# Performance work log

Hardware: AMD Instinct MI355X
Metric: run time of the kernel (lower is better)

Reference implementation:

```python
import jax, jax.numpy as jnp
import numpy as np

N_DRUG = 20000; N_DIS = 20000; E_G = 320000
B = 4096; N_MOL = 65536; E_MOL = 262144
IN = 128; H = 256; OUT = 128; NF = 9; V = 128
EPS = 1e-5


def _bn(x, g, b):
    # BatchNorm1d in training mode: batch statistics (biased var), eps=1e-5
    m = jnp.mean(x, 0); v = jnp.var(x, 0)
    return g * (x - m) * jax.lax.rsqrt(v + EPS) + b


def _gcn_conv(x, W, b, src, dst, n):
    # PyG GCNConv: add self-loops, sym-normalized aggregation of x@W, + bias
    h = x @ W  # [n, out]
    deg = jnp.ones((n,), x.dtype).at[dst].add(jnp.ones(src.shape, x.dtype))  # deg incl. self-loop
    dinv = jax.lax.rsqrt(deg)
    msg = (dinv[src] * dinv[dst])[:, None] * h[src]  # [E, out]
    out = (h / deg[:, None]).at[dst].add(msg)  # self-loop norm = 1/deg
    return out + b


def _gcn(x, Ws, bs, gs, betas, edge_index, n):
    src, dst = edge_index[0], edge_index[1]
    for i in range(len(Ws) - 1):
        x = jax.nn.relu(_bn(_gcn_conv(x, Ws[i], bs[i], src, dst, n), gs[i], betas[i]))
    return _gcn_conv(x, Ws[-1], bs[-1], src, dst, n)


def _conv_block(x, W, b, g, beta):
    # Conv1d(k=3,s=1,p=1) -> MaxPool1d(2,2) -> BatchNorm1d -> ReLU
    y = jax.lax.conv_general_dilated(x, W, (1,), ((1, 1),), dimension_numbers=('NCH', 'OIH', 'NCH')) + b[None, :, None]
    y = jax.lax.reduce_window(y, -jnp.inf, jax.lax.max, (1, 1, 2), (1, 1, 2), 'VALID')
    m = jnp.mean(y, (0, 2)); v = jnp.var(y, (0, 2))
    y = g[None, :, None] * (y - m[None, :, None]) * jax.lax.rsqrt(v + EPS)[None, :, None] + beta[None, :, None]
    return jax.nn.relu(y)


def setup_inputs() -> dict:
    key = jax.random.key(0)
    ks = iter(jax.random.split(key, 64))
    def nrm(shape, s=0.05):
        return jax.random.normal(next(ks), shape, jnp.float32) * s
    inp = {}
    inp['drug_x'] = nrm((N_DRUG, IN), 1.0)
    inp['drug_edge_index'] = jax.random.randint(next(ks), (2, E_G), 0, N_DRUG)
    inp['drug_idx'] = jax.random.randint(next(ks), (B,), 0, N_DRUG)
    inp['dis_x'] = nrm((N_DIS, IN), 1.0)
    inp['dis_edge_index'] = jax.random.randint(next(ks), (2, E_G), 0, N_DIS)
    inp['dis_idx'] = jax.random.randint(next(ks), (B,), 0, N_DIS)
    inp['mol_x'] = jax.random.randint(next(ks), (N_MOL, NF), 0, V)
    inp['mol_edge_index'] = jax.random.randint(next(ks), (2, E_MOL), 0, N_MOL)
    inp['mol_batch'] = jnp.sort(jax.random.randint(next(ks), (N_MOL,), 0, B))
    for p in ['dr', 'di']:
        inp[p + '_W0'] = nrm((IN, H)); inp[p + '_W1'] = nrm((H, H)); inp[p + '_W2'] = nrm((H, OUT))
        inp[p + '_b0'] = jnp.zeros((H,)); inp[p + '_b1'] = jnp.zeros((H,)); inp[p + '_b2'] = jnp.zeros((OUT,))
        inp[p + '_g0'] = jnp.ones((H,)); inp[p + '_g1'] = jnp.ones((H,))
        inp[p + '_be0'] = jnp.zeros((H,)); inp[p + '_be1'] = jnp.zeros((H,))
    inp['mol_emb'] = nrm((NF, V, H))
    inp['mo_W0'] = nrm((H, H)); inp['mo_W1'] = nrm((H, H)); inp['mo_W2'] = nrm((H, OUT))
    inp['mo_b0'] = jnp.zeros((H,)); inp['mo_b1'] = jnp.zeros((H,)); inp['mo_b2'] = jnp.zeros((OUT,))
    inp['mo_g0'] = jnp.ones((H,)); inp['mo_g1'] = jnp.ones((H,))
    inp['mo_be0'] = jnp.zeros((H,)); inp['mo_be1'] = jnp.zeros((H,))
    inp['c1_W'] = nrm((6, 3, 3), 0.2); inp['c1_b'] = jnp.zeros((6,)); inp['c1_g'] = jnp.ones((6,)); inp['c1_be'] = jnp.zeros((6,))
    inp['c2_W'] = nrm((6, 6, 3), 0.2); inp['c2_b'] = jnp.zeros((6,)); inp['c2_g'] = jnp.ones((6,)); inp['c2_be'] = jnp.zeros((6,))
    inp['l1_W'] = nrm((192, 128)); inp['l1_b'] = jnp.zeros((128,))
    inp['l2_W'] = nrm((128, 1)); inp['l2_b'] = jnp.zeros((1,))
    return inp


def reference(drug_x, drug_edge_index, drug_idx, dis_x, dis_edge_index, dis_idx, mol_x, mol_edge_index, mol_batch,
              dr_W0, dr_W1, dr_W2, dr_b0, dr_b1, dr_b2, dr_g0, dr_g1, dr_be0, dr_be1,
              di_W0, di_W1, di_W2, di_b0, di_b1, di_b2, di_g0, di_g1, di_be0, di_be1,
              mol_emb, mo_W0, mo_W1, mo_W2, mo_b0, mo_b1, mo_b2, mo_g0, mo_g1, mo_be0, mo_be1,
              c1_W, c1_b, c1_g, c1_be, c2_W, c2_b, c2_g, c2_be, l1_W, l1_b, l2_W, l2_b):
    dfeat = _gcn(drug_x, [dr_W0, dr_W1, dr_W2], [dr_b0, dr_b1, dr_b2], [dr_g0, dr_g1], [dr_be0, dr_be1], drug_edge_index, N_DRUG)
    sfeat = _gcn(dis_x, [di_W0, di_W1, di_W2], [di_b0, di_b1, di_b2], [di_g0, di_g1], [di_be0, di_be1], dis_edge_index, N_DIS)
    # AtomEncoder: sum of per-feature categorical embeddings -> [N_MOL, H]
    h = jnp.sum(mol_emb[jnp.arange(NF)[None, :], mol_x], axis=1)
    mfeat = _gcn(h, [mo_W0, mo_W1, mo_W2], [mo_b0, mo_b1, mo_b2], [mo_g0, mo_g1], [mo_be0, mo_be1], mol_edge_index, N_MOL)
    mpool = jax.ops.segment_sum(mfeat, mol_batch, num_segments=B)  # global_add_pool
    fea = jnp.concatenate([dfeat[drug_idx], mpool, sfeat[dis_idx]], axis=1).reshape(B, 3, OUT)
    fea = _conv_block(fea, c1_W, c1_b, c1_g, c1_be)
    fea = _conv_block(fea, c2_W, c2_b, c2_g, c2_be)
    fea = fea.reshape(B, -1)  # [B, 192]
    fea = jax.nn.relu(fea @ l1_W + l1_b)
    return fea @ l2_W + l2_b
```

## Files before the change

kernel.cpp:

```cpp
#include <hip/hip_runtime.h>
#include <hip/hip_bf16.h>

#define N_DRUG 20000
#define N_DIS  20000
#define E_G    320000
#define BATCH  4096
#define N_MOL  65536
#define E_MOL  262144
#define NF     9
#define NV     128
#define DH     256
#define SPAN_P 20096
#define NP     40192
#define NTOT   105728
#define ETOT   902144

typedef short s16x8 __attribute__((ext_vector_type(8)));
typedef unsigned short u16x8 __attribute__((ext_vector_type(8)));
typedef float f32x4 __attribute__((ext_vector_type(4)));

typedef __attribute__((address_space(1))) const void gvoid_t;
typedef __attribute__((address_space(3))) void lvoid_t;

__device__ __forceinline__ float bfu2f(unsigned short u) {
    return __uint_as_float(((unsigned int)u) << 16);
}
__device__ __forceinline__ unsigned short f2bfu(float f) {
    __hip_bfloat16 b = __float2bfloat16(f);
    return *reinterpret_cast<unsigned short*>(&b);
}
__device__ __forceinline__ void atomAddF(float* p, float v) { unsafeAtomicAdd(p, v); }

__global__ void k_sentinel(float* out, int n, float v) {
    int i = blockIdx.x * 256 + threadIdx.x;
    if (i < n) out[i] = v;
}

__global__ void k_cast_pair(const float* __restrict__ a, const float* __restrict__ b,
                            unsigned short* __restrict__ out) {
    int i4 = blockIdx.x * 256 + threadIdx.x;
    if (i4 >= NP * 32) return;
    int row = i4 >> 5, c4 = (i4 & 31) * 4;
    float4 v = {0.f, 0.f, 0.f, 0.f};
    if (row < N_DRUG) v = *reinterpret_cast<const float4*>(a + (size_t)row * 128 + c4);
    else if (row >= SPAN_P && row < SPAN_P + N_DIS)
        v = *reinterpret_cast<const float4*>(b + (size_t)(row - SPAN_P) * 128 + c4);
    ushort4 o = {f2bfu(v.x), f2bfu(v.y), f2bfu(v.z), f2bfu(v.w)};
    *reinterpret_cast<ushort4*>(out + (size_t)row * 128 + c4) = o;
}

__global__ void k_wcast3(const float* __restrict__ W0, const float* __restrict__ W1,
                         const float* __restrict__ W2,
                         unsigned short* __restrict__ T0, unsigned short* __restrict__ T1,
                         unsigned short* __restrict__ T2, int Cin) {
    int i = blockIdx.x * 256 + threadIdx.x;
    int t0 = Cin * 256, t1 = 256 * 256, t2 = 256 * 128;
    if (i < t0) {
        int k = i / 256, c = i - k * 256;
        T0[(size_t)c * Cin + k] = f2bfu(W0[i]);
    } else if (i < t0 + t1) {
        int e = i - t0;
        int k = e / 256, c = e - k * 256;
        T1[(size_t)c * 256 + k] = f2bfu(W1[e]);
    } else if (i < t0 + t1 + t2) {
        int e = i - t0 - t1;
        int k = e / 128, c = e - k * 128;
        T2[(size_t)c * 256 + k] = f2bfu(W2[e]);
    }
}

__global__ void k_count3(const int* __restrict__ eA, const int* __restrict__ eB,
                         const int* __restrict__ eC, int* __restrict__ cnt) {
    int e = blockIdx.x * 256 + threadIdx.x;
    if (e >= ETOT) return;
    int d;
    if (e < E_G) d = eA[E_G + e];
    else if (e < 2 * E_G) d = eB[E_G + (e - E_G)] + SPAN_P;
    else d = eC[E_MOL + (e - 2 * E_G)] + NP;
    atomicAdd(&cnt[d], 1);
}

__global__ void k_scan1(const int* __restrict__ cnt, int* __restrict__ rowStart,
                        int* __restrict__ bsum, float* __restrict__ dinv, int n) {
    __shared__ int sh[256];
    int i = blockIdx.x * 256 + threadIdx.x;
    int v = (i < n) ? cnt[i] : 0;
    if (i < n) dinv[i] = rsqrtf(1.0f + (float)v);
    sh[threadIdx.x] = v;
    __syncthreads();
    for (int off = 1; off < 256; off <<= 1) {
        int t = (threadIdx.x >= off) ? sh[threadIdx.x - off] : 0;
        __syncthreads();
        sh[threadIdx.x] += t;
        __syncthreads();
    }
    if (i < n) rowStart[i] = sh[threadIdx.x] - v;
    if (threadIdx.x == 255) bsum[blockIdx.x] = sh[255];
}
__global__ void k_scan2b(int* __restrict__ bsum, int nb) {
    __shared__ int sh[256];
    __shared__ int carry;
    int t = threadIdx.x;
    if (t == 0) carry = 0;
    __syncthreads();
    for (int c0 = 0; c0 < nb; c0 += 256) {
        int v = (c0 + t < nb) ? bsum[c0 + t] : 0;
        sh[t] = v;
        __syncthreads();
        for (int off = 1; off < 256; off <<= 1) {
            int u = (t >= off) ? sh[t - off] : 0;
            __syncthreads();
            sh[t] += u;
            __syncthreads();
        }
        if (c0 + t < nb) bsum[c0 + t] = carry + sh[t] - v;
        __syncthreads();
        if (t == 0) carry += sh[255];
        __syncthreads();
    }
}
__global__ void k_scan3(int* __restrict__ rowStart, int* __restrict__ cursor,
                        const int* __restrict__ bsum, int n, int E) {
    int i = blockIdx.x * 256 + threadIdx.x;
    if (i < n) {
        int r = rowStart[i] + bsum[blockIdx.x];
        rowStart[i] = r;
        cursor[i] = r;
    }
    if (i == 0) rowStart[n] = E;
}
__global__ void k_fill3(const int* __restrict__ eA, const int* __restrict__ eB,
                        const int* __restrict__ eC, const float* __restrict__ dinv,
                        int* __restrict__ cursor, int2* __restrict__ csr2) {
    int e = blockIdx.x * 256 + threadIdx.x;
    if (e >= ETOT) return;
    int s, d;
    if (e < E_G) { s = eA[e]; d = eA[E_G + e]; }
    else if (e < 2 * E_G) { int i = e - E_G; s = eB[i] + SPAN_P; d = eB[E_G + i] + SPAN_P; }
    else { int i = e - 2 * E_G; s = eC[i] + NP; d = eC[E_MOL + i] + NP; }
    int p = atomicAdd(&cursor[d], 1);
    csr2[p] = make_int2(s, __float_as_int(dinv[s] * dinv[d]));
}

template<int AFFINE, int STATS>
__global__ __launch_bounds__(256) void k_gemm_mfma(const unsigned short* __restrict__ A,
                                                   const unsigned short* __restrict__ Bt0,
                                                   const unsigned short* __restrict__ Bt1,
                                                   const unsigned short* __restrict__ Bt2,
                                                   const float* __restrict__ coef,
                                                   unsigned short* __restrict__ Cout,
                                                   float* __restrict__ bnbuf,
// ... 55 lines not shown
            }
        }
    };

    f32x4 acc[4][4];
#pragma unroll
    for (int fm = 0; fm < 4; ++fm)
#pragma unroll
        for (int fn = 0; fn < 4; ++fn) acc[fm][fn] = f32x4{0.f, 0.f, 0.f, 0.f};

    stage(0, 0);
    __syncthreads();
    int nk = Kg >> 5;
    for (int t = 0; t < nk; ++t) {
        int cur = t & 1;
        if (t + 1 < nk) stage(cur ^ 1, (t + 1) * 32);
        s16x8 a[4], b[4];
#pragma unroll
        for (int fm = 0; fm < 4; ++fm)
            a[fm] = *reinterpret_cast<const s16x8*>(&Al[cur][kg][wrow + fm * 16 + lr][0]);
        if (AFFINE) {
            int k0 = t * 32;
            float sc[8], sh[8];
#pragma unroll
            for (int e = 0; e < 8; ++e) {
                sc[e] = csc[k0 + kg * 8 + e];
                sh[e] = csh[k0 + kg * 8 + e];
            }
#pragma unroll
            for (int fm = 0; fm < 4; ++fm)
#pragma unroll
                for (int e = 0; e < 8; ++e) {
                    float f = bfu2f((unsigned short)a[fm][e]);
                    a[fm][e] = (short)f2bfu(fmaxf(fmaf(sc[e], f, sh[e]), 0.f));
                }
        }
#pragma unroll
        for (int fn = 0; fn < 4; ++fn)
            b[fn] = *reinterpret_cast<const s16x8*>(&Bl[cur][kg][wcol + fn * 16 + lr][0]);
#pragma unroll
        for (int fm = 0; fm < 4; ++fm)
#pragma unroll
            for (int fn = 0; fn < 4; ++fn)
                acc[fm][fn] = __builtin_amdgcn_mfma_f32_16x16x32_bf16(a[fm], b[fn], acc[fm][fn], 0, 0, 0);
        __syncthreads();
    }
#pragma unroll
    for (int fm = 0; fm < 4; ++fm)
#pragma unroll
        for (int r = 0; r < 4; ++r) {
            int row = bm + wrow + fm * 16 + kg * 4 + r;
#pragma unroll
            for (int fn = 0; fn < 4; ++fn) {
                int col = bn + wcol + fn * 16 + lr;
                Cout[(size_t)row * N + col] = f2bfu(acc[fm][fn][r]);
            }
        }
    if constexpr (STATS) {
        __shared__ float colS[128], colQ[128];
        if (tid < 128) { colS[tid] = 0.f; colQ[tid] = 0.f; }
        __syncthreads();
#pragma unroll
        for (int fn = 0; fn < 4; ++fn) {
            float s = 0.f, q = 0.f;
#pragma unroll
            for (int fm = 0; fm < 4; ++fm)
#pragma unroll
                for (int r = 0; r < 4; ++r) {
                    float v = acc[fm][fn][r];
                    s += v; q += v * v;
                }
            int cl = (w & 1) * 64 + fn * 16 + lr;
            atomicAdd(&colS[cl], s);
            atomicAdd(&colQ[cl], q);
        }
        __syncthreads();
        if (tid < 128) {
            atomAddF(&bnbuf[gs * 512 + bn + tid], colS[tid]);
            atomAddF(&bnbuf[gs * 512 + 256 + bn + tid], colQ[tid]);
        }
    }
}

template<int C, int BIAS, int OUTBF>
__global__ __launch_bounds__(256) void k_gather(const unsigned short* __restrict__ h,
                                                long long hoff,
                                                const float* __restrict__ dinv,
                                                const float* __restrict__ b0,
                                                const float* __restrict__ b1,
                                                const float* __restrict__ b2,
                                                const int2* __restrict__ csr2,
                                                const int* __restrict__ rowStart,
                                                void* __restrict__ outv, long long ooff,
                                                int rowoff, int rowend) {
    constexpr int PL = C / 32;
    int row = rowoff + blockIdx.x * 8 + (threadIdx.x >> 5);
    if (row >= rowend) return;
    int lane = threadIdx.x & 31;
    int c0 = lane * PL;

    auto loadRow = [&](int r, float* d) {
        const unsigned short* base = h + ((size_t)r * C - hoff) + c0;
        if constexpr (PL == 8) {
            u16x8 v = *reinterpret_cast<const u16x8*>(base);
#pragma unroll
            for (int e = 0; e < 8; ++e) d[e] = bfu2f((unsigned short)v[e]);
        } else {
            ushort4 v = *reinterpret_cast<const ushort4*>(base);
            d[0] = bfu2f(v.x); d[1] = bfu2f(v.y); d[2] = bfu2f(v.z); d[3] = bfu2f(v.w);
        }
    };

    float dd = dinv[row], ws = dd * dd;
    int beg = rowStart[row], end = rowStart[row + 1];
    float a0[PL], a1[PL], a2[PL], a3[PL];
    float t0[PL], t1[PL], t2[PL], t3[PL], t4[PL], t5[PL], t6[PL], t7[PL];
    loadRow(row, t0);
#pragma unroll
    for (int p = 0; p < PL; ++p) { a0[p] = t0[p] * ws; a1[p] = 0.f; a2[p] = 0.f; a3[p] = 0.f; }

    int j = beg;
    for (; j + 8 <= end; j += 8) {
        int2 e0 = csr2[j], e1 = csr2[j + 1], e2 = csr2[j + 2], e3 = csr2[j + 3];
        int2 e4 = csr2[j + 4], e5 = csr2[j + 5], e6 = csr2[j + 6], e7 = csr2[j + 7];
        float w0 = __int_as_float(e0.y), w1 = __int_as_float(e1.y);
        float w2 = __int_as_float(e2.y), w3 = __int_as_float(e3.y);
        float w4 = __int_as_float(e4.y), w5 = __int_as_float(e5.y);
        float w6 = __int_as_float(e6.y), w7 = __int_as_float(e7.y);
        loadRow(e0.x, t0); loadRow(e1.x, t1); loadRow(e2.x, t2); loadRow(e3.x, t3);
        loadRow(e4.x, t4); loadRow(e5.x, t5); loadRow(e6.x, t6); loadRow(e7.x, t7);
#pragma unroll
        for (int p = 0; p < PL; ++p) {
            a0[p] += w0 * t0[p]; a1[p] += w1 * t1[p];
            a2[p] += w2 * t2[p]; a3[p] += w3 * t3[p];
            a0[p] += w4 * t4[p]; a1[p] += w5 * t5[p];
            a2[p] += w6 * t6[p]; a3[p] += w7 * t7[p];
        }
    }
    for (; j + 4 <= end; j += 4) {
        int2 e0 = csr2[j], e1 = csr2[j + 1], e2 = csr2[j + 2], e3 = csr2[j + 3];
        float w0 = __int_as_float(e0.y), w1 = __int_as_float(e1.y);
        float w2 = __int_as_float(e2.y), w3 = __int_as_float(e3.y);
        loadRow(e0.x, t0); loadRow(e1.x, t1); loadRow(e2.x, t2); loadRow(e3.x, t3);
#pragma unroll
        for (int p = 0; p < PL; ++p) {
            a0[p] += w0 * t0[p]; a1[p] += w1 * t1[p];
            a2[p] += w2 * t2[p]; a3[p] += w3 * t3[p];
        }
    }
    for (; j < end; ++j) {
        int2 e0 = csr2[j];
        float w = __int_as_float(e0.y);
        loadRow(e0.x, t0);
#pragma unroll
        for (int p = 0; p < PL; ++p) a0[p] += w * t0[p];
    }
    const float* bp = nullptr;
    if (BIAS) bp = (row < SPAN_P) ? b0 : ((row < NP) ? b1 : b2);
#pragma unroll
    for (int p = 0; p < PL; ++p) {
        a0[p] += (a1[p] + a2[p]) + a3[p];
        if (BIAS) a0[p] += bp[c0 + p];
    }
    if constexpr (OUTBF) {
        unsigned short* o = (unsigned short*)outv + ((size_t)row * C - ooff) + c0;
        if constexpr (PL == 8) {
            u16x8 ov;
#pragma unroll
            for (int e = 0; e < 8; ++e) ov[e] = f2bfu(a0[e]);
            *reinterpret_cast<u16x8*>(o) = ov;
        } else {
            ushort4 ov = {f2bfu(a0[0]), f2bfu(a0[1]), f2bfu(a0[2]), f2bfu(a0[3])};
            *reinterpret_cast<ushort4*>(o) = ov;
        }
    } else {
        float* o = (float*)outv + ((size_t)row * C - ooff) + c0;
#pragma unroll
        for (int q = 0; q < PL / 4; ++q) {
            float4 ov = {a0[q * 4 + 0], a0[q * 4 + 1], a0[q * 4 + 2], a0[q * 4 + 3]};
            *reinterpret_cast<float4*>(o + q * 4) = ov;
        }
    }
}

__global__ __launch_bounds__(256) void k_bn_stats3(const unsigned short* __restrict__ x,
                                                   float* __restrict__ bnbuf) {
    __shared__ float smS[8][256];
    __shared__ float smQ[8][256];
    int t = threadIdx.x;
    int y = blockIdx.y;
    int off = (y < 2) ? y * SPAN_P : NP;
    int span = (y < 2) ? SPAN_P : N_MOL;
    int g = t >> 5;
    int lane = t & 31;
    int c0 = lane * 8;
    float s[8], q[8];
#pragma unroll
    for (int e = 0; e < 8; ++e) { s[e] = 0.f; q[e] = 0.f; }
    int stride = gridDim.x * 8;
    for (int r = blockIdx.x * 8 + g; r < span; r += stride) {
        u16x8 v = *reinterpret_cast<const u16x8*>(x + ((size_t)(off + r)) * 256 + c0);
#pragma unroll
        for (int e = 0; e < 8; ++e) {
            float f = bfu2f((unsigned short)v[e]);
            s[e] += f; q[e] += f * f;
        }
    }
#pragma unroll
    for (int e = 0; e < 8; ++e) { smS[g][c0 + e] = s[e]; smQ[g][c0 + e] = q[e]; }
    __syncthreads();
    float S = 0.f, Q = 0.f;
#pragma unroll
    for (int g2 = 0; g2 < 8; ++g2) { S += smS[g2][t]; Q += smQ[g2][t]; }
    atomAddF(&bnbuf[y * 512 + t], S);
    atomAddF(&bnbuf[y * 512 + 256 + t], Q);
}

__global__ void k_bn_coef3(float* __restrict__ bnbuf,
                           const float* __restrict__ g0, const float* __restrict__ be0,
                           const float* __restrict__ g1, const float* __restrict__ be1,
                           const float* __restrict__ g2, const float* __restrict__ be2,
                           float* __restrict__ coef, float invN01, float invN2) {
    int gg = blockIdx.x;
    int j = threadIdx.x;
    const float* gp = (gg == 0) ? g0 : ((gg == 1) ? g1 : g2);
    const float* bp = (gg == 0) ? be0 : ((gg == 1) ? be1 : be2);
    float invN = (gg < 2) ? invN01 : invN2;
    float* s = bnbuf + gg * 512;
    float m = s[j] * invN;
    float v = s[256 + j] * invN - m * m;
    float r = rsqrtf(fmaxf(v, 0.f) + 1e-5f);
    float sc = gp[j] * r;
    coef[gg * 512 + j] = sc;
    coef[gg * 512 + 256 + j] = bp[j] - m * sc;
    s[j] = 0.f;
    s[256 + j] = 0.f;
}

__global__ __launch_bounds__(256) void k_atom_enc(const int* __restrict__ mol_x,
                                                  const float* __restrict__ emb,
                                                  unsigned short* __restrict__ h) {
    __shared__ int sidx[4][NF];
    int t = threadIdx.x;
    if (t < 4 * NF) sidx[t / NF][t % NF] = mol_x[(blockIdx.x * 4 + t / NF) * NF + t % NF];
    __syncthreads();
    int r = t >> 6, lane = t & 63;
    int c0 = lane * 4;
    int row = blockIdx.x * 4 + r;
    float4 s = {0.f, 0.f, 0.f, 0.f};
#pragma unroll
    for (int f = 0; f < NF; ++f) {
        const float4 v = *reinterpret_cast<const float4*>(emb + ((size_t)f * NV + sidx[r][f]) * DH + c0);
        s.x += v.x; s.y += v.y; s.z += v.z; s.w += v.w;
    }
    ushort4 ov = {f2bfu(s.x), f2bfu(s.y), f2bfu(s.z), f2bfu(s.w)};
    *reinterpret_cast<ushort4*>(h + (size_t)row * DH + c0) = ov;
}

__global__ __launch_bounds__(128) void k_pool_seg_f(const float* __restrict__ mfeat,
                                                    const int* __restrict__ batch,
                                                    float* __restrict__ mpool) {
    __shared__ int sr[2];
    __shared__ float smS[8][128];
    int b = blockIdx.x, t = threadIdx.x;
    if (t < 2) {
        int target = b + t;
        int lo = 0, hi = N_MOL;
        while (lo < hi) {
            int mid = (lo + hi) >> 1;
            if (batch[mid] < target) lo = mid + 1; else hi = mid;
        }
        sr[t] = lo;
    }
    __syncthreads();
    int g = t >> 4;
    int lane = t & 15;
    int c0 = lane * 8;
    float s[8];
#pragma unroll
    for (int e = 0; e < 8; ++e) s[e] = 0.f;
    int e1 = sr[1];
    for (int i = sr[0] + g; i < e1; i += 8) {
        const float4 v0 = *reinterpret_cast<const float4*>(mfeat + (size_t)i * 128 + c0);
        const float4 v1 = *reinterpret_cast<const float4*>(mfeat + (size_t)i * 128 + c0 + 4);
        s[0] += v0.x; s[1] += v0.y; s[2] += v0.z; s[3] += v0.w;
        s[4] += v1.x; s[5] += v1.y; s[6] += v1.z; s[7] += v1.w;
    }
#pragma unroll
    for (int e = 0; e < 8; ++e) smS[g][c0 + e] = s[e];
    __syncthreads();
    float S = 0.f;
#pragma unroll
    for (int g2 = 0; g2 < 8; ++g2) S += smS[g2][t];
    mpool[(size_t)b * 128 + t] = S;
}

__global__ __launch_bounds__(64) void k_conv1(const float* __restrict__ dfeat,
                                              const float* __restrict__ mpool,
                                              const float* __restrict__ sfeat,
                                              const int* __restrict__ drug_idx,
                                              const int* __restrict__ dis_idx,
                                              const float* __restrict__ W,
                                              const float* __restrict__ bias,
                                              float* __restrict__ y1) {
    __shared__ float xs[3][128];
    __shared__ float w[54];
    __shared__ float bb[6];
    int b = blockIdx.x, t = threadIdx.x;
    int di = drug_idx[b], si = dis_idx[b];
    const float* r0 = dfeat + (size_t)di * 128;
    const float* r1 = mpool + (size_t)b * 128;
    const float* r2 = sfeat + (size_t)si * 128;
    xs[0][t] = r0[t]; xs[0][t + 64] = r0[t + 64];
    xs[1][t] = r1[t]; xs[1][t + 64] = r1[t + 64];
    xs[2][t] = r2[t]; xs[2][t + 64] = r2[t + 64];
    if (t < 54) w[t] = W[t];
    if (t < 6) bb[t] = bias[t];
    __syncthreads();
    int l0 = 2 * t, l1 = l0 + 1;
#pragma unroll
    for (int o = 0; o < 6; ++o) {
        float ya = bb[o], yb = bb[o];
#pragma unroll
        for (int i = 0; i < 3; ++i) {
            const float* wi = &w[(o * 3 + i) * 3];
            float xm1 = (l0 > 0) ? xs[i][l0 - 1] : 0.f;
            float x0 = xs[i][l0];
            float x1 = xs[i][l1];
            float x2 = (l1 < 127) ? xs[i][l1 + 1] : 0.f;
            ya += wi[0] * xm1 + wi[1] * x0 + wi[2] * x1;
            yb += wi[0] * x0 + wi[1] * x1 + wi[2] * x2;
        }
        y1[((size_t)b * 6 + o) * 64 + t] = fmaxf(ya, yb);
    }
}

__global__ __launch_bounds__(256) void k_head_stats(const float* __restrict__ y,
                                                    float* __restrict__ hb, int which, int L) {
    int o = blockIdx.x;
    int b0 = blockIdx.y * 256;
    int t = threadIdx.x;
    float s = 0.f, q = 0.f;
    int per = 256 * L;
    for (int idx = t; idx < per; idx += 256) {
        int b = b0 + idx / L;
        int l = idx - (idx / L) * L;
        float v = y[((size_t)b * 6 + o) * L + l];
        s += v; q += v * v;
    }
    __shared__ float sms[4], smq[4];
#pragma unroll
    for (int off = 32; off > 0; off >>= 1) {
        s += __shfl_down(s, off);
        q += __shfl_down(q, off);
    }
    if ((t & 63) == 0) { sms[t >> 6] = s; smq[t >> 6] = q; }
    __syncthreads();
    if (t == 0) {
        float S = 0.f, Q = 0.f;
        for (int i = 0; i < 4; ++i) { S += sms[i]; Q += smq[i]; }
        atomAddF(hb + which * 32 + o, S);
        atomAddF(hb + which * 32 + 8 + o, Q);
    }
}

__global__ void k_bn_fin(float* __restrict__ hb, int which, float invN) {
    int o = threadIdx.x;
    if (o >= 6) return;
    float* p = hb + which * 32;
    float m = p[o] * invN;
    float v = p[8 + o] * invN - m * m;
    p[16 + o] = m;
    p[24 + o] = rsqrtf(fmaxf(v, 0.f) + 1e-5f);
}

__global__ __launch_bounds__(64) void k_conv2(const float* __restrict__ y1,
                                              const float* __restrict__ hb,
                                              const float* __restrict__ g1,
                                              const float* __restrict__ be1,
                                              const float* __restrict__ W,
                                              const float* __restrict__ bias,
                                              float* __restrict__ y2) {
    __shared__ float xs[6][64];
    __shared__ float w[108];
    __shared__ float bb[6];
    int b = blockIdx.x, t = threadIdx.x;
    const float* mean = hb + 16;
    const float* rstd = hb + 24;
    for (int idx = t; idx < 384; idx += 64) {
        int o = idx >> 6, l = idx & 63;
        float v = y1[((size_t)b * 6 + o) * 64 + l];
        v = g1[o] * (v - mean[o]) * rstd[o] + be1[o];
        xs[o][l] = fmaxf(v, 0.f);
    }
    for (int idx = t; idx < 108; idx += 64) w[idx] = W[idx];
    if (t < 6) bb[t] = bias[t];
    __syncthreads();
    if (t >= 32) return;
    int l0 = 2 * t, l1 = l0 + 1;
#pragma unroll
    for (int o = 0; o < 6; ++o) {
        float ya = bb[o], yb = bb[o];
#pragma unroll
        for (int i = 0; i < 6; ++i) {
            const float* wi = &w[(o * 6 + i) * 3];
            float xm1 = (l0 > 0) ? xs[i][l0 - 1] : 0.f;
            float x0 = xs[i][l0];
            float x1 = xs[i][l1];
            float x2 = (l1 < 63) ? xs[i][l1 + 1] : 0.f;
            ya += wi[0] * xm1 + wi[1] * x0 + wi[2] * x1;
            yb += wi[0] * x0 + wi[1] * x1 + wi[2] * x2;
        }
        y2[((size_t)b * 6 + o) * 32 + t] = fmaxf(ya, yb);
    }
}

__global__ __launch_bounds__(128) void k_head(const float* __restrict__ y2,
                                              const float* __restrict__ hb,
                                              const float* __restrict__ g2,
                                              const float* __restrict__ be2,
                                              const float* __restrict__ l1W,
                                              const float* __restrict__ l1b,
                                              const float* __restrict__ l2W,
                                              const float* __restrict__ l2b,
                                              float* __restrict__ out) {
    __shared__ float fs[192];
    __shared__ float sm[2];
    int b = blockIdx.x, t = threadIdx.x;
    const float* mean = hb + 32 + 16;
    const float* rstd = hb + 32 + 24;
    for (int idx = t; idx < 192; idx += 128) {
        int o = idx >> 5, l = idx & 31;
        float v = y2[((size_t)b * 6 + o) * 32 + l];
        v = g2[o] * (v - mean[o]) * rstd[o] + be2[o];
        fs[idx] = fmaxf(v, 0.f);
    }
    __syncthreads();
    float h = l1b[t];
    for (int k = 0; k < 192; ++k)
        h += fs[k] * l1W[k * 128 + t];
    h = fmaxf(h, 0.f);
    float p = h * l2W[t];
#pragma unroll
    for (int off = 32; off > 0; off >>= 1) p += __shfl_down(p, off);
    if ((t & 63) == 0) sm[t >> 6] = p;
    __syncthreads();
    if (t == 0) out[b] = sm[0] + sm[1] + l2b[0];
}

extern "C" void kernel_launch(void* const* d_in, const int* in_sizes, int n_in,
                              void* d_out, int out_size, void* d_ws, size_t ws_size,
                              hipStream_t stream) {
    float* out = (float*)d_out;
    if (n_in != 52) { k_sentinel<<<16, 256, 0, stream>>>(out, out_size, -111.f); return; }
    if (in_sizes[0] != N_DRUG * 128 || in_sizes[29] != NF * NV * DH || in_sizes[48] != 192 * 128) {
        k_sentinel<<<16, 256, 0, stream>>>(out, out_size, -222.f); return;
    }

    char* w = (char*)d_ws;
    auto alloc = [&](size_t bytes) { char* p = w; w += (bytes + 255) & ~(size_t)255; return p; };
    unsigned short* B1 = (unsigned short*)alloc((size_t)NTOT * 256 * 2);
    unsigned short* B2 = (unsigned short*)alloc((size_t)NTOT * 256 * 2);
    float* fcat = (float*)B1;
    float* mpool = (float*)alloc((size_t)BATCH * 128 * 4);
    int*   cnt      = (int*)alloc((size_t)NTOT * 4);
    float* dinv     = (float*)alloc((size_t)NTOT * 4);
    int*   rowStart = (int*)alloc((size_t)(NTOT + 1) * 4);
    int*   cursor   = (int*)alloc((size_t)NTOT * 4);
    int2*  csr2     = (int2*)alloc((size_t)ETOT * 8);
    int*   bsum     = (int*)alloc(1024 * 4);
    float* bnbuf    = (float*)alloc(1536 * 4);
    float* coef     = (float*)alloc(1536 * 4);
    unsigned short* drT0 = (unsigned short*)alloc((size_t)128 * 256 * 2);
    unsigned short* drT1 = (unsigned short*)alloc((size_t)256 * 256 * 2);
    unsigned short* drT2 = (unsigned short*)alloc((size_t)256 * 128 * 2);
    unsigned short* diT0 = (unsigned short*)alloc((size_t)128 * 256 * 2);
    unsigned short* diT1 = (unsigned short*)alloc((size_t)256 * 256 * 2);
    unsigned short* diT2 = (unsigned short*)alloc((size_t)256 * 128 * 2);
    unsigned short* moT0 = (unsigned short*)alloc((size_t)256 * 256 * 2);
    unsigned short* moT1 = (unsigned short*)alloc((size_t)256 * 256 * 2);
    unsigned short* moT2 = (unsigned short*)alloc((size_t)256 * 128 * 2);
    float* hstat = (float*)alloc(64 * 4);
    float* y1    = (float*)alloc((size_t)BATCH * 6 * 64 * 4);
    float* y2    = (float*)alloc((size_t)BATCH * 6 * 32 * 4);
    if ((size_t)(w - (char*)d_ws) > ws_size) {
        k_sentinel<<<16, 256, 0, stream>>>(out, out_size, -333.f); return;
    }

    const float* drug_x  = (const float*)d_in[0];
    const int* drug_ei   = (const int*)d_in[1];
    const int* drug_idx  = (const int*)d_in[2];
    const float* dis_x   = (const float*)d_in[3];
    const int* dis_ei    = (const int*)d_in[4];
    const int* dis_idx   = (const int*)d_in[5];
    const int* mol_x     = (const int*)d_in[6];
    const int* mol_ei    = (const int*)d_in[7];
    const int* mol_b     = (const int*)d_in[8];
    const float *dr_W0 = (const float*)d_in[9], *dr_W1 = (const float*)d_in[10], *dr_W2 = (const float*)d_in[11];
    const float *dr_b2 = (const float*)d_in[14];
    const float *dr_g0 = (const float*)d_in[15], *dr_g1 = (const float*)d_in[16];
    const float *dr_be0 = (const float*)d_in[17], *dr_be1 = (const float*)d_in[18];
    const float *di_W0 = (const float*)d_in[19], *di_W1 = (const float*)d_in[20], *di_W2 = (const float*)d_in[21];
    const float *di_b2 = (const float*)d_in[24];
    const float *di_g0 = (const float*)d_in[25], *di_g1 = (const float*)d_in[26];
    const float *di_be0 = (const float*)d_in[27], *di_be1 = (const float*)d_in[28];
    const float* mol_emb = (const float*)d_in[29];
    const float *mo_W0 = (const float*)d_in[30], *mo_W1 = (const float*)d_in[31], *mo_W2 = (const float*)d_in[32];
    const float *mo_b2 = (const float*)d_in[35];
    const float *mo_g0 = (const float*)d_in[36], *mo_g1 = (const float*)d_in[37];
    const float *mo_be0 = (const float*)d_in[38], *mo_be1 = (const float*)d_in[39];
    const float *c1_W = (const float*)d_in[40], *c1_b = (const float*)d_in[41];
    const float *c1_g = (const float*)d_in[42], *c1_be = (const float*)d_in[43];
    const float *c2_W = (const float*)d_in[44], *c2_b = (const float*)d_in[45];
    const float *c2_g = (const float*)d_in[46], *c2_be = (const float*)d_in[47];
    const float *l1_W = (const float*)d_in[48], *l1_b = (const float*)d_in[49];
    const float *l2_W = (const float*)d_in[50], *l2_b = (const float*)d_in[51];

    const float invN01 = 1.0f / (float)N_DRUG;
    const float invNM  = 1.0f / (float)N_MOL;
    const long long MOFF = (long long)NP * 128;

    hipMemsetAsync(bnbuf, 0, 1536 * sizeof(float), stream);

    k_cast_pair<<<(NP * 32 + 255) / 256, 256, 0, stream>>>(drug_x, dis_x, B1);
    k_atom_enc<<<N_MOL / 4, 256, 0, stream>>>(mol_x, mol_emb, B1 + MOFF);

    hipMemsetAsync(cnt, 0, (size_t)NTOT * sizeof(int), stream);
    k_count3<<<(ETOT + 255) / 256, 256, 0, stream>>>(drug_ei, dis_ei, mol_ei, cnt);
    int nb = (NTOT + 255) / 256;
    k_scan1<<<nb, 256, 0, stream>>>(cnt, rowStart, bsum, dinv, NTOT);
    k_scan2b<<<1, 256, 0, stream>>>(bsum, nb);
    k_scan3<<<nb, 256, 0, stream>>>(rowStart, cursor, bsum, NTOT, ETOT);
    k_fill3<<<(ETOT + 255) / 256, 256, 0, stream>>>(drug_ei, dis_ei, mol_ei, dinv, cursor, csr2);

    int wt1 = 128 * 256 + 256 * 256 + 256 * 128;
    int wt2 = 256 * 256 + 256 * 256 + 256 * 128;
    k_wcast3<<<(wt1 + 255) / 256, 256, 0, stream>>>(dr_W0, dr_W1, dr_W2, drT0, drT1, drT2, 128);
    k_wcast3<<<(wt1 + 255) / 256, 256, 0, stream>>>(di_W0, di_W1, di_W2, diT0, diT1, diT2, 128);
    k_wcast3<<<(wt2 + 255) / 256, 256, 0, stream>>>(mo_W0, mo_W1, mo_W2, moT0, moT1, moT2, 256);

    k_gather<128, 0, 1><<<NP / 8, 256, 0, stream>>>(B1, 0, dinv, nullptr, nullptr, nullptr,
                                                    csr2, rowStart, B2, 0, 0, NP);
    k_gather<256, 0, 1><<<N_MOL / 8, 256, 0, stream>>>(B1, MOFF, dinv, nullptr, nullptr, nullptr,
                                                       csr2, rowStart, B2, MOFF, NP, NTOT);
    k_gemm_mfma<0, 1><<<dim3(2, 826), 256, 0, stream>>>(B2, drT0, diT0, moT0, nullptr,
        B1, bnbuf, 157, 314, SPAN_P, NP, N_DRUG, N_DIS, N_MOL, 0, 128, 256, MOFF, NP, 256);
    k_bn_coef3<<<3, 256, 0, stream>>>(bnbuf, dr_g0, dr_be0, di_g0, di_be0, mo_g0, mo_be0,
                                      coef, invN01, invNM);
    k_gemm_mfma<1, 0><<<dim3(2, 826), 256, 0, stream>>>(B1, drT1, diT1, moT1, coef,
        B2, nullptr, 157, 314, SPAN_P, NP, N_DRUG, N_DIS, N_MOL, 0, 256, 256, 0, 0, 256);
    k_gather<256, 0, 1><<<NTOT / 8, 256, 0, stream>>>(B2, 0, dinv, nullptr, nullptr, nullptr,
                                                      csr2, rowStart, B1, 0, 0, NTOT);
    k_bn_stats3<<<dim3(256, 3), 256, 0, stream>>>(B1, bnbuf);
    k_bn_coef3<<<3, 256, 0, stream>>>(bnbuf, dr_g1, dr_be1, di_g1, di_be1, mo_g1, mo_be1,
                                      coef, invN01, invNM);
    k_gemm_mfma<1, 0><<<dim3(1, 826), 256, 0, stream>>>(B1, drT2, diT2, moT2, coef,
        B2, nullptr, 157, 314, SPAN_P, NP, N_DRUG, N_DIS, N_MOL, 0, 256, 256, 0, 0, 128);
    k_gather<128, 1, 0><<<NTOT / 8, 256, 0, stream>>>(B2, 0, dinv, dr_b2, di_b2, mo_b2,
                                                      csr2, rowStart, fcat, 0, 0, NTOT);
    k_pool_seg_f<<<BATCH, 128, 0, stream>>>(fcat + (size_t)NP * 128, mol_b, mpool);

    const float* dfeat = fcat;
    const float* sfeat = fcat + (size_t)SPAN_P * 128;
    hipMemsetAsync(hstat, 0, 64 * 4, stream);
    k_conv1<<<BATCH, 64, 0, stream>>>(dfeat, mpool, sfeat, drug_idx, dis_idx, c1_W, c1_b, y1);
    k_head_stats<<<dim3(6, BATCH / 256), 256, 0, stream>>>(y1, hstat, 0, 64);
    k_bn_fin<<<1, 8, 0, stream>>>(hstat, 0, 1.0f / (BATCH * 64.0f));
    k_conv2<<<BATCH, 64, 0, stream>>>(y1, hstat, c1_g, c1_be, c2_W, c2_b, y2);
    k_head_stats<<<dim3(6, BATCH / 256), 256, 0, stream>>>(y2, hstat, 1, 32);
    k_bn_fin<<<1, 8, 0, stream>>>(hstat, 1, 1.0f / (BATCH * 32.0f));
    k_head<<<BATCH, 128, 0, stream>>>(y2, hstat, c2_g, c2_be, l1_W, l1_b, l2_W, l2_b, out);
}
```

Measured before the change: 558.7 us.

## Fuse prep kernels, fold BN stats into gather, gather only indexed drug/disease rows

Merges input casting with the atom encoder, and the three weight-cast launches into one. Folds the layer-1 BatchNorm statistics into the gather epilogue, using bucketed atomics in place of a separate stats pass. The final-layer gather now computes only the drug and disease rows selected by the batch indices plus all molecule rows, skipping about 32k unused node aggregations. This cuts launches and memory traffic, but the stats are now taken from bf16-rounded values and rely on each 8-row block falling inside a single graph span.

```diff
diff --git a/kernel.cpp b/kernel.cpp
--- a/kernel.cpp
+++ b/kernel.cpp
@@ -14,6 +14,7 @@
 #define NP     40192
 #define NTOT   105728
 #define ETOT   902144
+#define NBUCK  16
 
 typedef short s16x8 __attribute__((ext_vector_type(8)));
 typedef unsigned short u16x8 __attribute__((ext_vector_type(8)));
@@ -36,37 +37,65 @@
     if (i < n) out[i] = v;
 }
 
-__global__ void k_cast_pair(const float* __restrict__ a, const float* __restrict__ b,
-                            unsigned short* __restrict__ out) {
-    int i4 = blockIdx.x * 256 + threadIdx.x;
-    if (i4 >= NP * 32) return;
-    int row = i4 >> 5, c4 = (i4 & 31) * 4;
-    float4 v = {0.f, 0.f, 0.f, 0.f};
-    if (row < N_DRUG) v = *reinterpret_cast<const float4*>(a + (size_t)row * 128 + c4);
-    else if (row >= SPAN_P && row < SPAN_P + N_DIS)
-        v = *reinterpret_cast<const float4*>(b + (size_t)(row - SPAN_P) * 128 + c4);
-    ushort4 o = {f2bfu(v.x), f2bfu(v.y), f2bfu(v.z), f2bfu(v.w)};
-    *reinterpret_cast<ushort4*>(out + (size_t)row * 128 + c4) = o;
-}
-
-__global__ void k_wcast3(const float* __restrict__ W0, const float* __restrict__ W1,
-                         const float* __restrict__ W2,
-                         unsigned short* __restrict__ T0, unsigned short* __restrict__ T1,
-                         unsigned short* __restrict__ T2, int Cin) {
+__global__ __launch_bounds__(256) void k_in_prep(const float* __restrict__ a,
+                                                 const float* __restrict__ b,
+                                                 const int* __restrict__ mol_x,
+                                                 const float* __restrict__ emb,
+                                                 unsigned short* __restrict__ B1,
+                                                 unsigned short* __restrict__ molh) {
+    __shared__ int sidx[4][NF];
+    int bx = blockIdx.x, t = threadIdx.x;
+    if (bx < NP * 32 / 256) {
+        int i4 = bx * 256 + t;
+        int row = i4 >> 5, c4 = (i4 & 31) * 4;
+        float4 v = {0.f, 0.f, 0.f, 0.f};
+        if (row < N_DRUG) v = *reinterpret_cast<const float4*>(a + (size_t)row * 128 + c4);
+        else if (row >= SPAN_P && row < SPAN_P + N_DIS)
+            v = *reinterpret_cast<const float4*>(b + (size_t)(row - SPAN_P) * 128 + c4);
+        ushort4 o = {f2bfu(v.x), f2bfu(v.y), f2bfu(v.z), f2bfu(v.w)};
+        *reinterpret_cast<ushort4*>(B1 + (size_t)row * 128 + c4) = o;
+    } else {
+        int blk = bx - NP * 32 / 256;
+        if (t < 4 * NF) sidx[t / NF][t % NF] = mol_x[(blk * 4 + t / NF) * NF + t % NF];
+        __syncthreads();
+        int r = t >> 6, lane = t & 63;
+        int c0 = lane * 4;
+        int row = blk * 4 + r;
+        float4 s = {0.f, 0.f, 0.f, 0.f};
+#pragma unroll
+        for (int f = 0; f < NF; ++f) {
+            const float4 v = *reinterpret_cast<const float4*>(emb + ((size_t)f * NV + sidx[r][f]) * DH + c0);
+            s.x += v.x; s.y += v.y; s.z += v.z; s.w += v.w;
+        }
+        ushort4 ov = {f2bfu(s.x), f2bfu(s.y), f2bfu(s.z), f2bfu(s.w)};
+        *reinterpret_cast<ushort4*>(molh + (size_t)row * DH + c0) = ov;
+    }
+}
+
+__global__ void k_wcast9(const float* __restrict__ a0, const float* __restrict__ a1,
+                         const float* __restrict__ a2, const float* __restrict__ b0,
+                         const float* __restrict__ b1, const float* __restrict__ b2,
+                         const float* __restrict__ m0, const float* __restrict__ m1,
+                         const float* __restrict__ m2,
+                         unsigned short* __restrict__ A0, unsigned short* __restrict__ A1,
+                         unsigned short* __restrict__ A2, unsigned short* __restrict__ B0,
+                         unsigned short* __restrict__ B1, unsigned short* __restrict__ B2,
+                         unsigned short* __restrict__ M0, unsigned short* __restrict__ M1,
+                         unsigned short* __restrict__ M2) {
     int i = blockIdx.x * 256 + threadIdx.x;
-    int t0 = Cin * 256, t1 = 256 * 256, t2 = 256 * 128;
-    if (i < t0) {
-        int k = i / 256, c = i - k * 256;
-        T0[(size_t)c * Cin + k] = f2bfu(W0[i]);
-    } else if (i < t0 + t1) {
-        int e = i - t0;
-        int k = e / 256, c = e - k * 256;
-        T1[(size_t)c * 256 + k] = f2bfu(W1[e]);
-    } else if (i < t0 + t1 + t2) {
-        int e = i - t0 - t1;
-        int k = e / 128, c = e - k * 128;
-        T2[(size_t)c * 256 + k] = f2bfu(W2[e]);
-    }
+    const float* W; unsigned short* T; int K, N, e;
+    if (i < 32768)       { W = a0; T = A0; K = 128; N = 256; e = i; }
+    else if (i < 98304)  { W = a1; T = A1; K = 256; N = 256; e = i - 32768; }
+    else if (i < 131072) { W = a2; T = A2; K = 256; N = 128; e = i - 98304; }
+    else if (i < 163840) { W = b0; T = B0; K = 128; N = 256; e = i - 131072; }
+    else if (i < 229376) { W = b1; T = B1; K = 256; N = 256; e = i - 163840; }
+    else if (i < 262144) { W = b2; T = B2; K = 256; N = 128; e = i - 229376; }
+    else if (i < 327680) { W = m0; T = M0; K = 256; N = 256; e = i - 262144; }
+    else if (i < 393216) { W = m1; T = M1; K = 256; N = 256; e = i - 327680; }
+    else if (i < 425984) { W = m2; T = M2; K = 256; N = 128; e = i - 393216; }
+    else return;
+    int k = e / N, c = e - k * N;
+    T[(size_t)c * K + k] = f2bfu(W[e]);
 }
 
 __global__ void k_count3(const int* __restrict__ eA, const int* __restrict__ eB,
@@ -288,23 +317,17 @@
     }
 }
 
-template<int C, int BIAS, int OUTBF>
-__global__ __launch_bounds__(256) void k_gather(const unsigned short* __restrict__ h,
-                                                long long hoff,
-                                                const float* __restrict__ dinv,
-                                                const float* __restrict__ b0,
-                                                const float* __restrict__ b1,
-                                                const float* __restrict__ b2,
-                                                const int2* __restrict__ csr2,
-                                                const int* __restrict__ rowStart,
-                                                void* __restrict__ outv, long long ooff,
-                                                int rowoff, int rowend) {
+template<int C, int BIAS>
+__device__ __forceinline__ void gather_core(const unsigned short* __restrict__ h,
+                                            long long hoff,
+                                            const float* __restrict__ dinv,
+                                            const float* __restrict__ b0,
+                                            const float* __restrict__ b1,
+                                            const float* __restrict__ b2,
+                                            const int2* __restrict__ csr2,
+                                            const int* __restrict__ rowStart,
+                                            int row, int c0, float* a0) {
     constexpr int PL = C / 32;
-    int row = rowoff + blockIdx.x * 8 + (threadIdx.x >> 5);
-    if (row >= rowend) return;
-    int lane = threadIdx.x & 31;
-    int c0 = lane * PL;
-
     auto loadRow = [&](int r, float* d) {
         const unsigned short* base = h + ((size_t)r * C - hoff) + c0;
         if constexpr (PL == 8) {
@@ -316,15 +339,13 @@
             d[0] = bfu2f(v.x); d[1] = bfu2f(v.y); d[2] = bfu2f(v.z); d[3] = bfu2f(v.w);
         }
     };
-
     float dd = dinv[row], ws = dd * dd;
     int beg = rowStart[row], end = rowStart[row + 1];
-    float a0[PL], a1[PL], a2[PL], a3[PL];
+    float a1[PL], a2[PL], a3[PL];
     float t0[PL], t1[PL], t2[PL], t3[PL], t4[PL], t5[PL], t6[PL], t7[PL];
     loadRow(row, t0);
 #pragma unroll
     for (int p = 0; p < PL; ++p) { a0[p] = t0[p] * ws; a1[p] = 0.f; a2[p] = 0.f; a3[p] = 0.f; }
-
     int j = beg;
     for (; j + 8 <= end; j += 8) {
         int2 e0 = csr2[j], e1 = csr2[j + 1], e2 = csr2[j + 2], e3 = csr2[j + 3];
@@ -356,10 +377,10 @@
     }
     for (; j < end; ++j) {
         int2 e0 = csr2[j];
-        float w = __int_as_float(e0.y);
+        float ww = __int_as_float(e0.y);
         loadRow(e0.x, t0);
 #pragma unroll
-        for (int p = 0; p < PL; ++p) a0[p] += w * t0[p];
+        for (int p = 0; p < PL; ++p) a0[p] += ww * t0[p];
     }
     const float* bp = nullptr;
     if (BIAS) bp = (row < SPAN_P) ? b0 : ((row < NP) ? b1 : b2);
@@ -368,61 +389,109 @@
         a0[p] += (a1[p] + a2[p]) + a3[p];
         if (BIAS) a0[p] += bp[c0 + p];
     }
-    if constexpr (OUTBF) {
-        unsigned short* o = (unsigned short*)outv + ((size_t)row * C - ooff) + c0;
-        if constexpr (PL == 8) {
-            u16x8 ov;
-#pragma unroll
-            for (int e = 0; e < 8; ++e) ov[e] = f2bfu(a0[e]);
-            *reinterpret_cast<u16x8*>(o) = ov;
-        } else {
-            ushort4 ov = {f2bfu(a0[0]), f2bfu(a0[1]), f2bfu(a0[2]), f2bfu(a0[3])};
-            *reinterpret_cast<ushort4*>(o) = ov;
-        }
+}
+
+__global__ __launch_bounds__(256) void k_gather_l0(const unsigned short* __restrict__ B1,
+                                                   const float* __restrict__ dinv,
+                                                   const int2* __restrict__ csr2,
+                                                   const int* __restrict__ rowStart,
+                                                   unsigned short* __restrict__ B2,
+                                                   long long moff) {
+    int bx = blockIdx.x;
+    int grp = threadIdx.x >> 5;
+    int lane = threadIdx.x & 31;
+    if (bx < NP / 8) {
+        int row = bx * 8 + grp;
+        int c0 = lane * 4;
+        float a0[4];
+        gather_core<128, 0>(B1, 0, dinv, nullptr, nullptr, nullptr, csr2, rowStart, row, c0, a0);
+        ushort4 ov = {f2bfu(a0[0]), f2bfu(a0[1]), f2bfu(a0[2]), f2bfu(a0[3])};
+        *reinterpret_cast<ushort4*>(B2 + (size_t)row * 128 + c0) = ov;
     } else {
-        float* o = (float*)outv + ((size_t)row * C - ooff) + c0;
-#pragma unroll
-        for (int q = 0; q < PL / 4; ++q) {
-            float4 ov = {a0[q * 4 + 0], a0[q * 4 + 1], a0[q * 4 + 2], a0[q * 4 + 3]};
-            *reinterpret_cast<float4*>(o + q * 4) = ov;
-        }
-    }
-}
-
-__global__ __launch_bounds__(256) void k_bn_stats3(const unsigned short* __restrict__ x,
-                                                   float* __restrict__ bnbuf) {
+        int row = NP + (bx - NP / 8) * 8 + grp;
+        int c0 = lane * 8;
+        float a0[8];
+        gather_core<256, 0>(B1, moff, dinv, nullptr, nullptr, nullptr, csr2, rowStart, row, c0, a0);
+        u16x8 ov;
+#pragma unroll
+        for (int e = 0; e < 8; ++e) ov[e] = f2bfu(a0[e]);
+        *reinterpret_cast<u16x8*>(B2 + ((size_t)row * 256 - moff) + c0) = ov;
+    }
+}
+
+__global__ __launch_bounds__(256) void k_gather_l1s(const unsigned short* __restrict__ B2,
+                                                    const float* __restrict__ dinv,
+                                                    const int2* __restrict__ csr2,
+                                                    const int* __restrict__ rowStart,
+                                                    unsigned short* __restrict__ B1,
+                                                    float* __restrict__ bnpart) {
     __shared__ float smS[8][256];
     __shared__ float smQ[8][256];
+    int grp = threadIdx.x >> 5;
+    int lane = threadIdx.x & 31;
+    int row = blockIdx.x * 8 + grp;
+    int c0 = lane * 8;
+    float a0[8];
+    gather_core<256, 0>(B2, 0, dinv, nullptr, nullptr, nullptr, csr2, rowStart, row, c0, a0);
+    u16x8 ov;
+    float s8[8];
+#pragma unroll
+    for (int e = 0; e < 8; ++e) {
+        ov[e] = f2bfu(a0[e]);
+        s8[e] = bfu2f((unsigned short)ov[e]);
+    }
+    *reinterpret_cast<u16x8*>(B1 + (size_t)row * 256 + c0) = ov;
+#pragma unroll
+    for (int e = 0; e < 8; ++e) { smS[grp][c0 + e] = s8[e]; smQ[grp][c0 + e] = s8[e] * s8[e]; }
+    __syncthreads();
     int t = threadIdx.x;
-    int y = blockIdx.y;
-    int off = (y < 2) ? y * SPAN_P : NP;
-    int span = (y < 2) ? SPAN_P : N_MOL;
-    int g = t >> 5;
-    int lane = t & 31;
-    int c0 = lane * 8;
-    float s[8], q[8];
-#pragma unroll
-    for (int e = 0; e < 8; ++e) { s[e] = 0.f; q[e] = 0.f; }
-    int stride = gridDim.x * 8;
-    for (int r = blockIdx.x * 8 + g; r < span; r += stride) {
-        u16x8 v = *reinterpret_cast<const u16x8*>(x + ((size_t)(off + r)) * 256 + c0);
-#pragma unroll
-        for (int e = 0; e < 8; ++e) {
-            float f = bfu2f((unsigned short)v[e]);
-            s[e] += f; q[e] += f * f;
-        }
-    }
-#pragma unroll
-    for (int e = 0; e < 8; ++e) { smS[g][c0 + e] = s[e]; smQ[g][c0 + e] = q[e]; }
-    __syncthreads();
     float S = 0.f, Q = 0.f;
 #pragma unroll
     for (int g2 = 0; g2 < 8; ++g2) { S += smS[g2][t]; Q += smQ[g2][t]; }
-    atomAddF(&bnbuf[y * 512 + t], S);
-    atomAddF(&bnbuf[y * 512 + 256 + t], Q);
-}
-
-__global__ void k_bn_coef3(float* __restrict__ bnbuf,
+    int r0 = blockIdx.x * 8;
+    int g3 = (r0 < SPAN_P) ? 0 : ((r0 < NP) ? 1 : 2);
+    int bucket = blockIdx.x & (NBUCK - 1);
+    float* p = bnpart + ((size_t)g3 * NBUCK + bucket) * 512;
+    atomAddF(&p[t], S);
+    atomAddF(&p[256 + t], Q);
+}
+
+__global__ __launch_bounds__(256) void k_gather_idx(const unsigned short* __restrict__ h,
+                                                    const float* __restrict__ dinv,
+                                                    const float* __restrict__ dr_b,
+                                                    const float* __restrict__ di_b,
+                                                    const int* __restrict__ drug_idx,
+                                                    const int* __restrict__ dis_idx,
+                                                    const int2* __restrict__ csr2,
+                                                    const int* __restrict__ rowStart,
+                                                    float* __restrict__ outc) {
+    int slot = blockIdx.x * 8 + (threadIdx.x >> 5);
+    if (slot >= 2 * BATCH) return;
+    int row = (slot < BATCH) ? drug_idx[slot] : (dis_idx[slot - BATCH] + SPAN_P);
+    int lane = threadIdx.x & 31;
+    int c0 = lane * 4;
+    float a0[4];
+    gather_core<128, 1>(h, 0, dinv, dr_b, di_b, nullptr, csr2, rowStart, row, c0, a0);
+    float4 ov = {a0[0], a0[1], a0[2], a0[3]};
+    *reinterpret_cast<float4*>(outc + (size_t)slot * 128 + c0) = ov;
+}
+
+__global__ __launch_bounds__(256) void k_gather_mol(const unsigned short* __restrict__ h,
+                                                    const float* __restrict__ dinv,
+                                                    const float* __restrict__ mo_b,
+                                                    const int2* __restrict__ csr2,
+                                                    const int* __restrict__ rowStart,
+                                                    float* __restrict__ molf, long long moff) {
+    int row = NP + blockIdx.x * 8 + (threadIdx.x >> 5);
+    int lane = threadIdx.x & 31;
+    int c0 = lane * 4;
+    float a0[4];
+    gather_core<128, 1>(h, 0, dinv, nullptr, nullptr, mo_b, csr2, rowStart, row, c0, a0);
+    float4 ov = {a0[0], a0[1], a0[2], a0[3]};
+    *reinterpret_cast<float4*>(molf + ((size_t)row * 128 - moff) + c0) = ov;
+}
+
+__global__ void k_bn_coef3(const float* __restrict__ part, int nbuck,
                            const float* __restrict__ g0, const float* __restrict__ be0,
                            const float* __restrict__ g1, const float* __restrict__ be1,
                            const float* __restrict__ g2, const float* __restrict__ be2,
@@ -432,35 +501,18 @@
     const float* gp = (gg == 0) ? g0 : ((gg == 1) ? g1 : g2);
     const float* bp = (gg == 0) ? be0 : ((gg == 1) ? be1 : be2);
     float invN = (gg < 2) ? invN01 : invN2;
-    float* s = bnbuf + gg * 512;
-    float m = s[j] * invN;
-    float v = s[256 + j] * invN - m * m;
+    float S = 0.f, Q = 0.f;
+    for (int b = 0; b < nbuck; ++b) {
+        const float* p = part + ((size_t)gg * nbuck + b) * 512;
+        S += p[j];
+        Q += p[256 + j];
+    }
+    float m = S * invN;
+    float v = Q * invN - m * m;
     float r = rsqrtf(fmaxf(v, 0.f) + 1e-5f);
     float sc = gp[j] * r;
     coef[gg * 512 + j] = sc;
     coef[gg * 512 + 256 + j] = bp[j] - m * sc;
-    s[j] = 0.f;
-    s[256 + j] = 0.f;
-}
-
-__global__ __launch_bounds__(256) void k_atom_enc(const int* __restrict__ mol_x,
-                                                  const float* __restrict__ emb,
-                                                  unsigned short* __restrict__ h) {
-    __shared__ int sidx[4][NF];
-    int t = threadIdx.x;
-    if (t < 4 * NF) sidx[t / NF][t % NF] = mol_x[(blockIdx.x * 4 + t / NF) * NF + t % NF];
-    __syncthreads();
-    int r = t >> 6, lane = t & 63;
-    int c0 = lane * 4;
-    int row = blockIdx.x * 4 + r;
-    float4 s = {0.f, 0.f, 0.f, 0.f};
-#pragma unroll
-    for (int f = 0; f < NF; ++f) {
-        const float4 v = *reinterpret_cast<const float4*>(emb + ((size_t)f * NV + sidx[r][f]) * DH + c0);
-        s.x += v.x; s.y += v.y; s.z += v.z; s.w += v.w;
-    }
-    ushort4 ov = {f2bfu(s.x), f2bfu(s.y), f2bfu(s.z), f2bfu(s.w)};
-    *reinterpret_cast<ushort4*>(h + (size_t)row * DH + c0) = ov;
 }
 
 __global__ __launch_bounds__(128) void k_pool_seg_f(const float* __restrict__ mfeat,
@@ -501,11 +553,8 @@
     mpool[(size_t)b * 128 + t] = S;
 }
 
-__global__ __launch_bounds__(64) void k_conv1(const float* __restrict__ dfeat,
+__global__ __launch_bounds__(64) void k_conv1(const float* __restrict__ dgs,
                                               const float* __restrict__ mpool,
-                                              const float* __restrict__ sfeat,
-                                              const int* __restrict__ drug_idx,
-                                              const int* __restrict__ dis_idx,
                                               const float* __restrict__ W,
                                               const float* __restrict__ bias,
                                               float* __restrict__ y1) {
@@ -513,10 +562,9 @@
     __shared__ float w[54];
     __shared__ float bb[6];
     int b = blockIdx.x, t = threadIdx.x;
-    int di = drug_idx[b], si = dis_idx[b];
-    const float* r0 = dfeat + (size_t)di * 128;
+    const float* r0 = dgs + (size_t)b * 128;
     const float* r1 = mpool + (size_t)b * 128;
-    const float* r2 = sfeat + (size_t)si * 128;
+    const float* r2 = dgs + (size_t)(BATCH + b) * 128;
     xs[0][t] = r0[t]; xs[0][t + 64] = r0[t + 64];
     xs[1][t] = r1[t]; xs[1][t + 64] = r1[t + 64];
     xs[2][t] = r2[t]; xs[2][t + 64] = r2[t + 64];
@@ -667,7 +715,8 @@
     auto alloc = [&](size_t bytes) { char* p = w; w += (bytes + 255) & ~(size_t)255; return p; };
     unsigned short* B1 = (unsigned short*)alloc((size_t)NTOT * 256 * 2);
     unsigned short* B2 = (unsigned short*)alloc((size_t)NTOT * 256 * 2);
-    float* fcat = (float*)B1;
+    float* molf = (float*)B1;
+    float* dgs  = molf + (size_t)N_MOL * 128;
     float* mpool = (float*)alloc((size_t)BATCH * 128 * 4);
     int*   cnt      = (int*)alloc((size_t)NTOT * 4);
     float* dinv     = (float*)alloc((size_t)NTOT * 4);
@@ -676,6 +725,7 @@
     int2*  csr2     = (int2*)alloc((size_t)ETOT * 8);
     int*   bsum     = (int*)alloc(1024 * 4);
     float* bnbuf    = (float*)alloc(1536 * 4);
+    float* bnpart   = (float*)alloc((size_t)3 * NBUCK * 512 * 4);
     float* coef     = (float*)alloc(1536 * 4);
     unsigned short* drT0 = (unsigned short*)alloc((size_t)128 * 256 * 2);
     unsigned short* drT1 = (unsigned short*)alloc((size_t)256 * 256 * 2);
@@ -726,10 +776,10 @@
     const float invNM  = 1.0f / (float)N_MOL;
     const long long MOFF = (long long)NP * 128;
 
-    hipMemsetAsync(bnbuf, 0, 1536 * sizeof(float), stream);
-
-    k_cast_pair<<<(NP * 32 + 255) / 256, 256, 0, stream>>>(drug_x, dis_x, B1);
-    k_atom_enc<<<N_MOL / 4, 256, 0, stream>>>(mol_x, mol_emb, B1 + MOFF);
+    hipMemsetAsync(bnbuf, 0, (1536 + (size_t)3 * NBUCK * 512) * sizeof(float), stream);
+
+    k_in_prep<<<NP * 32 / 256 + N_MOL / 4, 256, 0, stream>>>(drug_x, dis_x, mol_x, mol_emb,
+                                                             B1, B1 + MOFF);
 
     hipMemsetAsync(cnt, 0, (size_t)NTOT * sizeof(int), stream);
     k_count3<<<(ETOT + 255) / 256, 256, 0, stream>>>(drug_ei, dis_ei, mol_ei, cnt);
@@ -739,37 +789,30 @@
     k_scan3<<<nb, 256, 0, stream>>>(rowStart, cursor, bsum, NTOT, ETOT);
     k_fill3<<<(ETOT + 255) / 256, 256, 0, stream>>>(drug_ei, dis_ei, mol_ei, dinv, cursor, csr2);
 
-    int wt1 = 128 * 256 + 256 * 256 + 256 * 128;
-    int wt2 = 256 * 256 + 256 * 256 + 256 * 128;
-    k_wcast3<<<(wt1 + 255) / 256, 256, 0, stream>>>(dr_W0, dr_W1, dr_W2, drT0, drT1, drT2, 128);
-    k_wcast3<<<(wt1 + 255) / 256, 256, 0, stream>>>(di_W0, di_W1, di_W2, diT0, diT1, diT2, 128);
-    k_wcast3<<<(wt2 + 255) / 256, 256, 0, stream>>>(mo_W0, mo_W1, mo_W2, moT0, moT1, moT2, 256);
-
-    k_gather<128, 0, 1><<<NP / 8, 256, 0, stream>>>(B1, 0, dinv, nullptr, nullptr, nullptr,
-                                                    csr2, rowStart, B2, 0, 0, NP);
-    k_gather<256, 0, 1><<<N_MOL / 8, 256, 0, stream>>>(B1, MOFF, dinv, nullptr, nullptr, nullptr,
-                                                       csr2, rowStart, B2, MOFF, NP, NTOT);
+    k_wcast9<<<(425984 + 255) / 256, 256, 0, stream>>>(dr_W0, dr_W1, dr_W2, di_W0, di_W1, di_W2,
+                                                       mo_W0, mo_W1, mo_W2,
+                                                       drT0, drT1, drT2, diT0, diT1, diT2,
+                                                       moT0, moT1, moT2);
+
+    k_gather_l0<<<NTOT / 8, 256, 0, stream>>>(B1, dinv, csr2, rowStart, B2, MOFF);
     k_gemm_mfma<0, 1><<<dim3(2, 826), 256, 0, stream>>>(B2, drT0, diT0, moT0, nullptr,
         B1, bnbuf, 157, 314, SPAN_P, NP, N_DRUG, N_DIS, N_MOL, 0, 128, 256, MOFF, NP, 256);
-    k_bn_coef3<<<3, 256, 0, stream>>>(bnbuf, dr_g0, dr_be0, di_g0, di_be0, mo_g0, mo_be0,
+    k_bn_coef3<<<3, 256, 0, stream>>>(bnbuf, 1, dr_g0, dr_be0, di_g0, di_be0, mo_g0, mo_be0,
                                       coef, invN01, invNM);
     k_gemm_mfma<1, 0><<<dim3(2, 826), 256, 0, stream>>>(B1, drT1, diT1, moT1, coef,
         B2, nullptr, 157, 314, SPAN_P, NP, N_DRUG, N_DIS, N_MOL, 0, 256, 256, 0, 0, 256);
-    k_gather<256, 0, 1><<<NTOT / 8, 256, 0, stream>>>(B2, 0, dinv, nullptr, nullptr, nullptr,
-                                                      csr2, rowStart, B1, 0, 0, NTOT);
-    k_bn_stats3<<<dim3(256, 3), 256, 0, stream>>>(B1, bnbuf);
-    k_bn_coef3<<<3, 256, 0, stream>>>(bnbuf, dr_g1, dr_be1, di_g1, di_be1, mo_g1, mo_be1,
+    k_gather_l1s<<<NTOT / 8, 256, 0, stream>>>(B2, dinv, csr2, rowStart, B1, bnpart);
+    k_bn_coef3<<<3, 256, 0, stream>>>(bnpart, NBUCK, dr_g1, dr_be1, di_g1, di_be1, mo_g1, mo_be1,
                                       coef, invN01, invNM);
     k_gemm_mfma<1, 0><<<dim3(1, 826), 256, 0, stream>>>(B1, drT2, diT2, moT2, coef,
         B2, nullptr, 157, 314, SPAN_P, NP, N_DRUG, N_DIS, N_MOL, 0, 256, 256, 0, 0, 128);
-    k_gather<128, 1, 0><<<NTOT / 8, 256, 0, stream>>>(B2, 0, dinv, dr_b2, di_b2, mo_b2,
-                                                      csr2, rowStart, fcat, 0, 0, NTOT);
-    k_pool_seg_f<<<BATCH, 128, 0, stream>>>(fcat + (size_t)NP * 128, mol_b, mpool);
-
-    const float* dfeat = fcat;
-    const float* sfeat = fcat + (size_t)SPAN_P * 128;
+    k_gather_idx<<<2 * BATCH / 8, 256, 0, stream>>>(B2, dinv, dr_b2, di_b2, drug_idx, dis_idx,
+                                                    csr2, rowStart, dgs);
+    k_gather_mol<<<N_MOL / 8, 256, 0, stream>>>(B2, dinv, mo_b2, csr2, rowStart, molf, MOFF);
+    k_pool_seg_f<<<BATCH, 128, 0, stream>>>(molf, mol_b, mpool);
+
     hipMemsetAsync(hstat, 0, 64 * 4, stream);
-    k_conv1<<<BATCH, 64, 0, stream>>>(dfeat, mpool, sfeat, drug_idx, dis_idx, c1_W, c1_b, y1);
+    k_conv1<<<BATCH, 64, 0, stream>>>(dgs, mpool, c1_W, c1_b, y1);
     k_head_stats<<<dim3(6, BATCH / 256), 256, 0, stream>>>(y1, hstat, 0, 64);
     k_bn_fin<<<1, 8, 0, stream>>>(hstat, 0, 1.0f / (BATCH * 64.0f));
     k_conv2<<<BATCH, 64, 0, stream>>>(y1, hstat, c1_g, c1_be, c2_W, c2_b, y2);
```

Result: faster. 540.3 us (-3.3%).
